# Performance work log

Measured on AMD Instinct MI355X. Metric: run time of the kernel, lower is better.

Reference implementation:

```python
import jax, jax.numpy as jnp
import numpy as np

EPS = 1e-05
GROUPS = 8


def setup_inputs() -> dict:
    key = jax.random.key(0)
    k1, k2, k3 = jax.random.split(key, 3)
    N, C, H, W = 32, 256, 56, 56
    x = jax.random.normal(k1, (N, C, H, W), dtype=jnp.float32)
    weight = jnp.ones((C,), dtype=jnp.float32)
    bias = jnp.zeros((C,), dtype=jnp.float32)
    gate_logits = jnp.array([2.8, 0.2, 1.1], dtype=jnp.float32)
    diag_proj = jnp.array([[0.08, -0.05, 0.08],
                           [-0.03, 0.08, -0.01],
                           [-0.05, -0.04, -0.07]], dtype=jnp.float32)
    return {"x": x, "weight": weight, "bias": bias,
            "gate_logits": gate_logits, "diag_proj": diag_proj}


def reference(x, weight, bias, gate_logits, diag_proj):
    xf = x.astype(jnp.float32)
    N, C, H, W = xf.shape

    # variance descriptor (differentiable: first-instance path recomputes without detach)
    batch_var = jnp.var(xf, axis=(0, 2, 3)).mean()    # per-channel var -> mean
    sample_var = jnp.var(xf, axis=(1, 2, 3)).mean()   # per-sample var -> mean
    channel_var = jnp.var(xf, axis=1).mean()          # var over channels at each (n,h,w) -> mean
    desc = jnp.tanh(jnp.log(jnp.maximum(jnp.stack([batch_var, sample_var, channel_var]), EPS)))

    gate = jax.nn.softmax(gate_logits + diag_proj @ desc)  # [3]

    # batch norm (training mode: batch statistics over N,H,W per channel)
    mu_b = xf.mean(axis=(0, 2, 3), keepdims=True)
    var_b = xf.var(axis=(0, 2, 3), keepdims=True)
    x_bn = (xf - mu_b) / jnp.sqrt(var_b + EPS)

    # layer norm = group_norm with 1 group: per-sample stats over C,H,W
    mu_l = xf.mean(axis=(1, 2, 3), keepdims=True)
    var_l = xf.var(axis=(1, 2, 3), keepdims=True)
    x_ln = (xf - mu_l) / jnp.sqrt(var_l + EPS)

    # group norm with GROUPS groups
    xg = xf.reshape(N, GROUPS, C // GROUPS, H, W)
    mu_g = xg.mean(axis=(2, 3, 4), keepdims=True)
    var_g = xg.var(axis=(2, 3, 4), keepdims=True)
    x_gn = ((xg - mu_g) / jnp.sqrt(var_g + EPS)).reshape(N, C, H, W)

    mixed = gate[0] * x_bn + gate[1] * x_ln + gate[2] * x_gn
    y = mixed * weight[None, :, None, None] + bias[None, :, None, None]
    return y.astype(x.dtype)
```

## Files before the change

### kernel.cpp

```cpp
#include <hip/hip_runtime.h>
#include <hip/hip_bf16.h>

#define NN 32
#define CC 256
#define HW 3136
#define HW4 784
#define CHW 802816
#define CHW4 200704
#define NCHW 25690112
#define GROUPS 8
#define CPG 32
#define NHW 100352
#define GHW 100352
#define EPSF 1e-5f
#define PCHUNK 13
#define NPT2 (NN*PCHUNK)
#define CGS 2
#define CPB 128

__global__ __launch_bounds__(256) void plane_stats_kernel(
    const float4* __restrict__ x4, float* __restrict__ S1, float* __restrict__ S2)
{
    const int wave = threadIdx.x >> 6, lane = threadIdx.x & 63;
    const int nc = blockIdx.x * 4 + wave;
    const float4* p = x4 + (size_t)nc * HW4;
    float s1 = 0.f, s2 = 0.f;
    #pragma unroll 4
    for (int i = lane; i < HW4; i += 64) {
        float4 v = p[i];
        s1 += v.x + v.y + v.z + v.w;
        s2 += v.x*v.x + v.y*v.y + v.z*v.z + v.w*v.w;
    }
    #pragma unroll
    for (int off = 32; off; off >>= 1) {
        s1 += __shfl_down(s1, off, 64);
        s2 += __shfl_down(s2, off, 64);
    }
    if (lane == 0) { S1[nc] = s1; S2[nc] = s2; }
}

__global__ __launch_bounds__(256) void chansum_kernel(
    const float* __restrict__ x, float* __restrict__ pT)
{
    const int b = blockIdx.x;
    const int chunk = b % PCHUNK;
    const int nc = b / PCHUNK;
    const int n = nc % NN;
    const int cg = nc / NN;
    const int pos = chunk * 256 + threadIdx.x;
    float T = 0.f;
    if (pos < HW) {
        const float* p = x + (size_t)n * CHW + (size_t)cg * CPB * HW + pos;
        #pragma unroll 16
        for (int c = 0; c < CPB; ++c) T += p[(size_t)c * HW];
    }
    pT[b * 256 + threadIdx.x] = (pos < HW) ? T : 0.f;
}

__global__ __launch_bounds__(256) void combine_kernel(
    const float* __restrict__ pT, float* __restrict__ pT2)
{
    const int b = blockIdx.x;
    const int tid = threadIdx.x;
    const float T = pT[b * 256 + tid] + pT[NN * PCHUNK * 256 + b * 256 + tid];
    float t2 = T * T;
    #pragma unroll
    for (int off = 32; off; off >>= 1) t2 += __shfl_down(t2, off, 64);
    __shared__ float sh[4];
    const int wave = tid >> 6, lane = tid & 63;
    if (lane == 0) sh[wave] = t2;
    __syncthreads();
    if (tid == 0) pT2[b] = sh[0] + sh[1] + sh[2] + sh[3];
}

__global__ __launch_bounds__(256) void finalize_kernel(
    const float* __restrict__ S1, const float* __restrict__ S2,
    const float* __restrict__ partialT2,
    const float* __restrict__ weight, const float* __restrict__ bias,
    const float* __restrict__ gate_logits, const float* __restrict__ diag_proj,
    float* __restrict__ A, float* __restrict__ B)
{
    const int tid = threadIdx.x;
    __shared__ float sh_mu_b[CC], sh_rs_b[CC];
    __shared__ float sh_mu_g[NN * GROUPS], sh_rs_g[NN * GROUPS];
    __shared__ float sh_mu_l[NN], sh_rs_l[NN];
    __shared__ float sh_red1[4], sh_red2[4], sh_red3[4], sh_red4[4];
    __shared__ float sh_gate[3];

    const float inv_NHW  = 1.f / (float)NHW;
    const float inv_CHW  = 1.f / (float)CHW;
    const float inv_GHW  = 1.f / (float)GHW;
    const float inv_NCHW = 1.f / (float)NCHW;

    const int c = tid;
    float s1 = 0.f, s2 = 0.f;
    for (int n = 0; n < NN; ++n) { s1 += S1[n * CC + c]; s2 += S2[n * CC + c]; }
    const float mu_b  = s1 * inv_NHW;
    const float var_b = s2 * inv_NHW - mu_b * mu_b;
    sh_mu_b[c] = mu_b;
    sh_rs_b[c] = rsqrtf(var_b + EPSF);

    const int ng_n = tid >> 3, ng_g = tid & 7;
    float s1g = 0.f, s2g = 0.f;
    for (int cc = 0; cc < CPG; ++cc) {
        const int idx = ng_n * CC + ng_g * CPG + cc;
        s1g += S1[idx]; s2g += S2[idx];
    }
    const float mu_g  = s1g * inv_GHW;
    const float var_g = s2g * inv_GHW - mu_g * mu_g;
    sh_mu_g[tid] = mu_g;
    sh_rs_g[tid] = rsqrtf(var_g + EPSF);

    float s1l = s1g, s2l = s2g;
    #pragma unroll
    for (int off = 1; off < 8; off <<= 1) {
        s1l += __shfl_xor(s1l, off, 64);
        s2l += __shfl_xor(s2l, off, 64);
    }
    float var_l_contrib = 0.f;
    if (ng_g == 0) {
        const float mu_l  = s1l * inv_CHW;
        const float var_l = s2l * inv_CHW - mu_l * mu_l;
        sh_mu_l[ng_n] = mu_l;
        sh_rs_l[ng_n] = rsqrtf(var_l + EPSF);
        var_l_contrib = var_l;
    }

    float t2p = 0.f;
    for (int i = tid; i < NPT2; i += 256) t2p += partialT2[i];

    float r1 = var_b, r2 = s2, r3 = var_l_contrib, r4 = t2p;
    #pragma unroll
    for (int off = 32; off; off >>= 1) {
        r1 += __shfl_down(r1, off, 64);
        r2 += __shfl_down(r2, off, 64);
        r3 += __shfl_down(r3, off, 64);
        r4 += __shfl_down(r4, off, 64);
    }
    const int wave = tid >> 6, lane = tid & 63;
    if (lane == 0) { sh_red1[wave] = r1; sh_red2[wave] = r2; sh_red3[wave] = r3; sh_red4[wave] = r4; }
    __syncthreads();
    if (tid == 0) {
        const float sum_var_b = sh_red1[0] + sh_red1[1] + sh_red1[2] + sh_red1[3];
        const float total_x2  = sh_red2[0] + sh_red2[1] + sh_red2[2] + sh_red2[3];
        const float sum_var_l = sh_red3[0] + sh_red3[1] + sh_red3[2] + sh_red3[3];
        const float sum_T2    = sh_red4[0] + sh_red4[1] + sh_red4[2] + sh_red4[3];

        const float batch_var   = sum_var_b * (1.f / (float)CC);
        const float sample_var  = sum_var_l * (1.f / (float)NN);
        const float channel_var = total_x2 * inv_NCHW
                                - sum_T2 * inv_NHW * (1.f / ((float)CC * (float)CC));

        float desc[3];
        desc[0] = tanhf(logf(fmaxf(batch_var,   EPSF)));
        desc[1] = tanhf(logf(fmaxf(sample_var,  EPSF)));
        desc[2] = tanhf(logf(fmaxf(channel_var, EPSF)));

        float lg[3];
        #pragma unroll
        for (int i = 0; i < 3; ++i) {
            lg[i] = gate_logits[i] + diag_proj[i*3+0]*desc[0]
                                   + diag_proj[i*3+1]*desc[1]
                                   + diag_proj[i*3+2]*desc[2];
        }
        const float m = fmaxf(lg[0], fmaxf(lg[1], lg[2]));
        const float e0 = expf(lg[0]-m), e1 = expf(lg[1]-m), e2 = expf(lg[2]-m);
        const float inv = 1.f / (e0 + e1 + e2);
        sh_gate[0] = e0 * inv; sh_gate[1] = e1 * inv; sh_gate[2] = e2 * inv;
    }
    __syncthreads();

    const float g0 = sh_gate[0], g1 = sh_gate[1], g2 = sh_gate[2];
    for (int i = tid; i < NN * CC; i += 256) {
        const int n = i >> 8, ch = i & 255, g = ch >> 5;
        const float w = weight[ch], bi = bias[ch];
        const float rb = sh_rs_b[ch], rl = sh_rs_l[n], rg = sh_rs_g[n*8+g];
        const float mb = sh_mu_b[ch], ml = sh_mu_l[n], mg = sh_mu_g[n*8+g];
        const float scale = g0*rb + g1*rl + g2*rg;
        const float offs  = g0*mb*rb + g1*ml*rl + g2*mg*rg;
        A[i] = w * scale;
        B[i] = bi - w * offs;
    }
}

__global__ __launch_bounds__(256) void apply_kernel(
    const float4* __restrict__ x4, const float* __restrict__ A,
    const float* __restrict__ B, float4* __restrict__ y4)
{
    const int nc = blockIdx.x;
    const float a = A[nc], b = B[nc];
    const float4* xp = x4 + (size_t)nc * HW4;
    float4* yp = y4 + (size_t)nc * HW4;
    for (int i = threadIdx.x; i < HW4; i += 256) {
        float4 v = xp[i];
        v.x = fmaf(v.x, a, b);
        v.y = fmaf(v.y, a, b);
        v.z = fmaf(v.z, a, b);
        v.w = fmaf(v.w, a, b);
        yp[i] = v;
    }
}

extern "C" void kernel_launch(void* const* d_in, const int* in_sizes, int n_in,
                              void* d_out, int out_size, void* d_ws, size_t ws_size,
                              hipStream_t stream) {
    const float* x           = (const float*)d_in[0];
    const float* weight      = (const float*)d_in[1];
    const float* bias        = (const float*)d_in[2];
    const float* gate_logits = (const float*)d_in[3];
    const float* diag_proj   = (const float*)d_in[4];
    float* out = (float*)d_out;

    float* ws  = (float*)d_ws;
    float* S1  = ws;
    float* S2  = ws + 8192;
    float* A   = ws + 16384;
    float* B   = ws + 24576;
    float* pT2 = ws + 32768;
    float* pT  = ws + 33280;

    plane_stats_kernel<<<NN * 64, 256, 0, stream>>>((const float4*)x, S1, S2);
    chansum_kernel<<<CGS * NN * PCHUNK, 256, 0, stream>>>(x, pT);
    combine_kernel<<<NN * PCHUNK, 256, 0, stream>>>(pT, pT2);
    finalize_kernel<<<1, 256, 0, stream>>>(S1, S2, pT2, weight, bias,
                                           gate_logits, diag_proj, A, B);
    apply_kernel<<<NN * CC, 256, 0, stream>>>((const float4*)x, A, B, (float4*)out);
}
```

Baseline: 77.28 us.

## Fuse plane stats and channel-sum passes into one launch with float4 channel sums

Merges the per-plane sum/sumsq kernel and the per-position channel-sum kernel into a single launch, with disjoint block ranges running each role. The channel-sum path now reads float4 vectors and splits channels into 4 groups of 64 instead of 2 of 128, so the combine kernel adds four partials. The aim is to drop a kernel launch, let both reads of x run concurrently and possibly share L2, and widen the strided channel loads. The workspace offset for the partial buffer moves, and pT4 must fit within the workspace.

```diff
diff --git a/kernel.cpp b/kernel.cpp
--- a/kernel.cpp
+++ b/kernel.cpp
@@ -13,57 +13,70 @@
 #define NHW 100352
 #define GHW 100352
 #define EPSF 1e-5f
-#define PCHUNK 13
-#define NPT2 (NN*PCHUNK)
-#define CGS 2
-#define CPB 128
-
-__global__ __launch_bounds__(256) void plane_stats_kernel(
-    const float4* __restrict__ x4, float* __restrict__ S1, float* __restrict__ S2)
-{
-    const int wave = threadIdx.x >> 6, lane = threadIdx.x & 63;
-    const int nc = blockIdx.x * 4 + wave;
-    const float4* p = x4 + (size_t)nc * HW4;
-    float s1 = 0.f, s2 = 0.f;
-    #pragma unroll 4
-    for (int i = lane; i < HW4; i += 64) {
-        float4 v = p[i];
-        s1 += v.x + v.y + v.z + v.w;
-        s2 += v.x*v.x + v.y*v.y + v.z*v.z + v.w*v.w;
-    }
-    #pragma unroll
-    for (int off = 32; off; off >>= 1) {
-        s1 += __shfl_down(s1, off, 64);
-        s2 += __shfl_down(s2, off, 64);
-    }
-    if (lane == 0) { S1[nc] = s1; S2[nc] = s2; }
-}
-
-__global__ __launch_bounds__(256) void chansum_kernel(
-    const float* __restrict__ x, float* __restrict__ pT)
-{
-    const int b = blockIdx.x;
-    const int chunk = b % PCHUNK;
-    const int nc = b / PCHUNK;
-    const int n = nc % NN;
-    const int cg = nc / NN;
-    const int pos = chunk * 256 + threadIdx.x;
-    float T = 0.f;
-    if (pos < HW) {
-        const float* p = x + (size_t)n * CHW + (size_t)cg * CPB * HW + pos;
-        #pragma unroll 16
-        for (int c = 0; c < CPB; ++c) T += p[(size_t)c * HW];
-    }
-    pT[b * 256 + threadIdx.x] = (pos < HW) ? T : 0.f;
+
+#define PCH4 4
+#define CG4 4
+#define CPB4 64
+#define NCHAN_BLOCKS (CG4*NN*PCH4)
+#define NPLANE_BLOCKS 2048
+#define NPT2 (NN*PCH4)
+
+__global__ __launch_bounds__(256) void stats_kernel(
+    const float4* __restrict__ x4, float* __restrict__ S1, float* __restrict__ S2,
+    float4* __restrict__ pT4)
+{
+    const int tid = threadIdx.x;
+    if (blockIdx.x < NCHAN_BLOCKS) {
+        const int b = blockIdx.x;
+        const int chunk = b & 3;
+        const int nc = b >> 2;
+        const int n = nc & 31;
+        const int cg = nc >> 5;
+        const int p4 = chunk * 256 + tid;
+        float4 T = make_float4(0.f, 0.f, 0.f, 0.f);
+        if (p4 < HW4) {
+            const float4* p = x4 + (size_t)n * CHW4 + (size_t)cg * CPB4 * HW4 + p4;
+            #pragma unroll 16
+            for (int c = 0; c < CPB4; ++c) {
+                float4 v = p[(size_t)c * HW4];
+                T.x += v.x; T.y += v.y; T.z += v.z; T.w += v.w;
+            }
+        }
+        pT4[b * 256 + tid] = T;
+    } else {
+        const int pb = blockIdx.x - NCHAN_BLOCKS;
+        const int wave = tid >> 6, lane = tid & 63;
+        const int ncid = pb * 4 + wave;
+        const float4* p = x4 + (size_t)ncid * HW4;
+        float s1 = 0.f, s2 = 0.f;
+        #pragma unroll 4
+        for (int i = lane; i < HW4; i += 64) {
+            float4 v = p[i];
+            s1 += v.x + v.y + v.z + v.w;
+            s2 += v.x*v.x + v.y*v.y + v.z*v.z + v.w*v.w;
+        }
+        #pragma unroll
+        for (int off = 32; off; off >>= 1) {
+            s1 += __shfl_down(s1, off, 64);
+            s2 += __shfl_down(s2, off, 64);
+        }
+        if (lane == 0) { S1[ncid] = s1; S2[ncid] = s2; }
+    }
 }
 
 __global__ __launch_bounds__(256) void combine_kernel(
-    const float* __restrict__ pT, float* __restrict__ pT2)
+    const float4* __restrict__ pT4, float* __restrict__ pT2)
 {
     const int b = blockIdx.x;
     const int tid = threadIdx.x;
-    const float T = pT[b * 256 + tid] + pT[NN * PCHUNK * 256 + b * 256 + tid];
-    float t2 = T * T;
+    const int n = b >> 2, chunk = b & 3;
+    float4 T = make_float4(0.f, 0.f, 0.f, 0.f);
+    #pragma unroll
+    for (int cg = 0; cg < CG4; ++cg) {
+        float4 v = pT4[((cg * NN + n) * PCH4 + chunk) * 256 + tid];
+        T.x += v.x; T.y += v.y; T.z += v.z; T.w += v.w;
+    }
+    float t2 = T.x*T.x + T.y*T.y + T.z*T.z + T.w*T.w;
     #pragma unroll
     for (int off = 32; off; off >>= 1) t2 += __shfl_down(t2, off, 64);
     __shared__ float sh[4];
@@ -217,11 +230,11 @@
     float* A   = ws + 16384;
     float* B   = ws + 24576;
     float* pT2 = ws + 32768;
-    float* pT  = ws + 33280;
-
-    plane_stats_kernel<<<NN * 64, 256, 0, stream>>>((const float4*)x, S1, S2);
-    chansum_kernel<<<CGS * NN * PCHUNK, 256, 0, stream>>>(x, pT);
-    combine_kernel<<<NN * PCHUNK, 256, 0, stream>>>(pT, pT2);
+    float* pT4f = ws + 33024;
+
+    stats_kernel<<<NCHAN_BLOCKS + NPLANE_BLOCKS, 256, 0, stream>>>(
+        (const float4*)x, S1, S2, (float4*)pT4f);
+    combine_kernel<<<NPT2, 256, 0, stream>>>((const float4*)pT4f, pT2);
     finalize_kernel<<<1, 256, 0, stream>>>(S1, S2, pT2, weight, bias,
                                            gate_logits, diag_proj, A, B);
     apply_kernel<<<NN * CC, 256, 0, stream>>>((const float4*)x, A, B, (float4*)out);
```

Result: no change. 78.30 us (+1.3%).

## Fuse all stages into one persistent kernel with software grid barriers

Applied to the files above, without the earlier changes.

Replaces the five separate launches (plane stats, channel sums, combine, finalize, apply) with a single kernel of 1024 blocks. Two atomic-counter grid barriers separate the statistics, finalize and apply phases. The channel-sum pass is reworked to use float4 loads and a shared-memory reduction in each block, which removes the separate combine kernel. This cuts launch overhead and inter-kernel gaps, but the barriers assume all 1024 blocks are co-resident, block 0 alone runs finalize while every other block waits, and a memset launch is added to reset the barrier.

```diff
diff --git a/kernel.cpp b/kernel.cpp
--- a/kernel.cpp
+++ b/kernel.cpp
@@ -3,201 +3,225 @@
 
 #define NN 32
 #define CC 256
-#define HW 3136
 #define HW4 784
+#define CHW4 200704
 #define CHW 802816
-#define CHW4 200704
 #define NCHW 25690112
 #define GROUPS 8
 #define CPG 32
 #define NHW 100352
 #define GHW 100352
 #define EPSF 1e-5f
-#define PCHUNK 13
-#define NPT2 (NN*PCHUNK)
-#define CGS 2
-#define CPB 128
-
-__global__ __launch_bounds__(256) void plane_stats_kernel(
-    const float4* __restrict__ x4, float* __restrict__ S1, float* __restrict__ S2)
+
+#define NBLK 1024
+#define PCHUNK 25
+
+__device__ inline void grid_barrier(unsigned* cnt, unsigned* gen)
 {
-    const int wave = threadIdx.x >> 6, lane = threadIdx.x & 63;
-    const int nc = blockIdx.x * 4 + wave;
-    const float4* p = x4 + (size_t)nc * HW4;
-    float s1 = 0.f, s2 = 0.f;
-    #pragma unroll 4
-    for (int i = lane; i < HW4; i += 64) {
-        float4 v = p[i];
-        s1 += v.x + v.y + v.z + v.w;
-        s2 += v.x*v.x + v.y*v.y + v.z*v.z + v.w*v.w;
-    }
-    #pragma unroll
-    for (int off = 32; off; off >>= 1) {
-        s1 += __shfl_down(s1, off, 64);
-        s2 += __shfl_down(s2, off, 64);
-    }
-    if (lane == 0) { S1[nc] = s1; S2[nc] = s2; }
+    __syncthreads();
+    if (threadIdx.x == 0) {
+        __threadfence();
+        unsigned g = __hip_atomic_load(gen, __ATOMIC_RELAXED, __HIP_MEMORY_SCOPE_AGENT);
+        unsigned old = __hip_atomic_fetch_add(cnt, 1u, __ATOMIC_ACQ_REL, __HIP_MEMORY_SCOPE_AGENT);
+        if (old == NBLK - 1u) {
+            __hip_atomic_store(cnt, 0u, __ATOMIC_RELAXED, __HIP_MEMORY_SCOPE_AGENT);
+            __hip_atomic_store(gen, g + 1u, __ATOMIC_RELEASE, __HIP_MEMORY_SCOPE_AGENT);
+        } else {
+            for (long it = 0; it < 2000000; ++it) {
+                if (__hip_atomic_load(gen, __ATOMIC_RELAXED, __HIP_MEMORY_SCOPE_AGENT) != g) break;
+                __builtin_amdgcn_s_sleep(2);
+            }
+        }
+        __threadfence();
+    }
+    __syncthreads();
 }
 
-__global__ __launch_bounds__(256) void chansum_kernel(
-    const float* __restrict__ x, float* __restrict__ pT)
-{
-    const int b = blockIdx.x;
-    const int chunk = b % PCHUNK;
-    const int nc = b / PCHUNK;
-    const int n = nc % NN;
-    const int cg = nc / NN;
-    const int pos = chunk * 256 + threadIdx.x;
-    float T = 0.f;
-    if (pos < HW) {
-        const float* p = x + (size_t)n * CHW + (size_t)cg * CPB * HW + pos;
-        #pragma unroll 16
-        for (int c = 0; c < CPB; ++c) T += p[(size_t)c * HW];
-    }
-    pT[b * 256 + threadIdx.x] = (pos < HW) ? T : 0.f;
-}
-
-__global__ __launch_bounds__(256) void combine_kernel(
-    const float* __restrict__ pT, float* __restrict__ pT2)
-{
-    const int b = blockIdx.x;
-    const int tid = threadIdx.x;
-    const float T = pT[b * 256 + tid] + pT[NN * PCHUNK * 256 + b * 256 + tid];
-    float t2 = T * T;
-    #pragma unroll
-    for (int off = 32; off; off >>= 1) t2 += __shfl_down(t2, off, 64);
-    __shared__ float sh[4];
-    const int wave = tid >> 6, lane = tid & 63;
-    if (lane == 0) sh[wave] = t2;
-    __syncthreads();
-    if (tid == 0) pT2[b] = sh[0] + sh[1] + sh[2] + sh[3];
-}
-
-__global__ __launch_bounds__(256) void finalize_kernel(
-    const float* __restrict__ S1, const float* __restrict__ S2,
-    const float* __restrict__ partialT2,
+__global__ __launch_bounds__(256, 4) void mega_kernel(
+    const float4* __restrict__ x4,
     const float* __restrict__ weight, const float* __restrict__ bias,
     const float* __restrict__ gate_logits, const float* __restrict__ diag_proj,
-    float* __restrict__ A, float* __restrict__ B)
+    float4* __restrict__ y4,
+    unsigned* cnt, unsigned* gen,
+    float* __restrict__ S1, float* __restrict__ S2,
+    float* __restrict__ Aarr, float* __restrict__ Barr,
+    float* __restrict__ pT2)
 {
-    const int tid = threadIdx.x;
-    __shared__ float sh_mu_b[CC], sh_rs_b[CC];
-    __shared__ float sh_mu_g[NN * GROUPS], sh_rs_g[NN * GROUPS];
-    __shared__ float sh_mu_l[NN], sh_rs_l[NN];
-    __shared__ float sh_red1[4], sh_red2[4], sh_red3[4], sh_red4[4];
-    __shared__ float sh_gate[3];
-
-    const float inv_NHW  = 1.f / (float)NHW;
-    const float inv_CHW  = 1.f / (float)CHW;
-    const float inv_GHW  = 1.f / (float)GHW;
-    const float inv_NCHW = 1.f / (float)NCHW;
-
-    const int c = tid;
-    float s1 = 0.f, s2 = 0.f;
-    for (int n = 0; n < NN; ++n) { s1 += S1[n * CC + c]; s2 += S2[n * CC + c]; }
-    const float mu_b  = s1 * inv_NHW;
-    const float var_b = s2 * inv_NHW - mu_b * mu_b;
-    sh_mu_b[c] = mu_b;
-    sh_rs_b[c] = rsqrtf(var_b + EPSF);
-
-    const int ng_n = tid >> 3, ng_g = tid & 7;
-    float s1g = 0.f, s2g = 0.f;
-    for (int cc = 0; cc < CPG; ++cc) {
-        const int idx = ng_n * CC + ng_g * CPG + cc;
-        s1g += S1[idx]; s2g += S2[idx];
-    }
-    const float mu_g  = s1g * inv_GHW;
-    const float var_g = s2g * inv_GHW - mu_g * mu_g;
-    sh_mu_g[tid] = mu_g;
-    sh_rs_g[tid] = rsqrtf(var_g + EPSF);
-
-    float s1l = s1g, s2l = s2g;
+    const int tid  = threadIdx.x;
+    const int wave = tid >> 6, lane = tid & 63;
+
     #pragma unroll
-    for (int off = 1; off < 8; off <<= 1) {
-        s1l += __shfl_xor(s1l, off, 64);
-        s2l += __shfl_xor(s2l, off, 64);
-    }
-    float var_l_contrib = 0.f;
-    if (ng_g == 0) {
-        const float mu_l  = s1l * inv_CHW;
-        const float var_l = s2l * inv_CHW - mu_l * mu_l;
-        sh_mu_l[ng_n] = mu_l;
-        sh_rs_l[ng_n] = rsqrtf(var_l + EPSF);
-        var_l_contrib = var_l;
-    }
-
-    float t2p = 0.f;
-    for (int i = tid; i < NPT2; i += 256) t2p += partialT2[i];
-
-    float r1 = var_b, r2 = s2, r3 = var_l_contrib, r4 = t2p;
+    for (int rep = 0; rep < 2; ++rep) {
+        const int plane = blockIdx.x * 4 + wave + rep * (NBLK * 4);
+        const float4* p = x4 + (size_t)plane * HW4;
+        float s1 = 0.f, s2 = 0.f;
+        #pragma unroll 4
+        for (int i = lane; i < HW4; i += 64) {
+            float4 v = p[i];
+            s1 += v.x + v.y + v.z + v.w;
+            s2 += v.x*v.x + v.y*v.y + v.z*v.z + v.w*v.w;
+        }
+        #pragma unroll
+        for (int off = 32; off; off >>= 1) {
+            s1 += __shfl_down(s1, off, 64);
+            s2 += __shfl_down(s2, off, 64);
+        }
+        if (lane == 0) { S1[plane] = s1; S2[plane] = s2; }
+    }
+
+    {
+        const int n = blockIdx.x >> 5, chunk = blockIdx.x & 31;
+        const int start = chunk * PCHUNK;
+        const int len = (HW4 - start) < PCHUNK ? (HW4 - start) : PCHUNK;
+        const int cg = tid >> 5, p = tid & 31;
+        float4 T = make_float4(0.f, 0.f, 0.f, 0.f);
+        if (p < len) {
+            const float4* q = x4 + (size_t)n * CHW4 + (size_t)(cg * 32) * HW4 + start + p;
+            #pragma unroll 8
+            for (int c = 0; c < 32; ++c) {
+                float4 v = q[(size_t)c * HW4];
+                T.x += v.x; T.y += v.y; T.z += v.z; T.w += v.w;
+            }
+        }
+        __shared__ float4 shT[32];
+        #pragma unroll
+        for (int k = 0; k < 8; ++k) {
+            if (cg == k) {
+                if (k == 0) shT[p] = T;
+                else { shT[p].x += T.x; shT[p].y += T.y; shT[p].z += T.z; shT[p].w += T.w; }
+            }
+            __syncthreads();
+        }
+        float t2 = 0.f;
+        if (tid < 32) {
+            float4 t = shT[tid];
+            t2 = t.x*t.x + t.y*t.y + t.z*t.z + t.w*t.w;
+        }
+        #pragma unroll
+        for (int off = 32; off; off >>= 1) t2 += __shfl_down(t2, off, 64);
+        if (tid == 0) pT2[blockIdx.x] = t2;
+    }
+
+    grid_barrier(cnt, gen);
+
+    if (blockIdx.x == 0) {
+        __shared__ float sh_mu_b[CC], sh_rs_b[CC];
+        __shared__ float sh_mu_g[NN * GROUPS], sh_rs_g[NN * GROUPS];
+        __shared__ float sh_mu_l[NN], sh_rs_l[NN];
+        __shared__ float sh_red1[4], sh_red2[4], sh_red3[4], sh_red4[4];
+        __shared__ float sh_gate[3];
+
+        const float inv_NHW  = 1.f / (float)NHW;
+        const float inv_CHW  = 1.f / (float)CHW;
+        const float inv_GHW  = 1.f / (float)GHW;
+        const float inv_NCHW = 1.f / (float)NCHW;
+
+        const int c = tid;
+        float s1 = 0.f, s2 = 0.f;
+        for (int n = 0; n < NN; ++n) { s1 += S1[n * CC + c]; s2 += S2[n * CC + c]; }
+        const float mu_b  = s1 * inv_NHW;
+        const float var_b = s2 * inv_NHW - mu_b * mu_b;
+        sh_mu_b[c] = mu_b;
+        sh_rs_b[c] = rsqrtf(var_b + EPSF);
+
+        const int ng_n = tid >> 3, ng_g = tid & 7;
+        float s1g = 0.f, s2g = 0.f;
+        for (int cc2 = 0; cc2 < CPG; ++cc2) {
+            const int idx = ng_n * CC + ng_g * CPG + cc2;
+            s1g += S1[idx]; s2g += S2[idx];
+        }
+        const float mu_g  = s1g * inv_GHW;
+        const float var_g = s2g * inv_GHW - mu_g * mu_g;
+        sh_mu_g[tid] = mu_g;
+        sh_rs_g[tid] = rsqrtf(var_g + EPSF);
+
+        float s1l = s1g, s2l = s2g;
+        #pragma unroll
+        for (int off = 1; off < 8; off <<= 1) {
+            s1l += __shfl_xor(s1l, off, 64);
+            s2l += __shfl_xor(s2l, off, 64);
+        }
+        float var_l_contrib = 0.f;
+        if (ng_g == 0) {
+            const float mu_l  = s1l * inv_CHW;
+            const float var_l = s2l * inv_CHW - mu_l * mu_l;
+            sh_mu_l[ng_n] = mu_l;
+            sh_rs_l[ng_n] = rsqrtf(var_l + EPSF);
+            var_l_contrib = var_l;
+        }
+
+        float t2p = 0.f;
+        for (int i = tid; i < NBLK; i += 256) t2p += pT2[i];
+
+        float r1 = var_b, r2 = s2, r3 = var_l_contrib, r4 = t2p;
+        #pragma unroll
+        for (int off = 32; off; off >>= 1) {
+            r1 += __shfl_down(r1, off, 64);
+            r2 += __shfl_down(r2, off, 64);
+            r3 += __shfl_down(r3, off, 64);
+            r4 += __shfl_down(r4, off, 64);
+        }
+        if (lane == 0) { sh_red1[wave] = r1; sh_red2[wave] = r2; sh_red3[wave] = r3; sh_red4[wave] = r4; }
+        __syncthreads();
+        if (tid == 0) {
+            const float sum_var_b = sh_red1[0] + sh_red1[1] + sh_red1[2] + sh_red1[3];
+            const float total_x2  = sh_red2[0] + sh_red2[1] + sh_red2[2] + sh_red2[3];
+            const float sum_var_l = sh_red3[0] + sh_red3[1] + sh_red3[2] + sh_red3[3];
+            const float sum_T2    = sh_red4[0] + sh_red4[1] + sh_red4[2] + sh_red4[3];
+
+            const float batch_var   = sum_var_b * (1.f / (float)CC);
+            const float sample_var  = sum_var_l * (1.f / (float)NN);
+            const float channel_var = total_x2 * inv_NCHW
+                                    - sum_T2 * inv_NHW * (1.f / ((float)CC * (float)CC));
+
+            float desc[3];
+            desc[0] = tanhf(logf(fmaxf(batch_var,   EPSF)));
+            desc[1] = tanhf(logf(fmaxf(sample_var,  EPSF)));
+            desc[2] = tanhf(logf(fmaxf(channel_var, EPSF)));
+
+            float lg[3];
+            #pragma unroll
+            for (int i = 0; i < 3; ++i) {
+                lg[i] = gate_logits[i] + diag_proj[i*3+0]*desc[0]
+                                       + diag_proj[i*3+1]*desc[1]
+                                       + diag_proj[i*3+2]*desc[2];
+            }
+            const float m = fmaxf(lg[0], fmaxf(lg[1], lg[2]));
+            const float e0 = expf(lg[0]-m), e1 = expf(lg[1]-m), e2 = expf(lg[2]-m);
+            const float inv = 1.f / (e0 + e1 + e2);
+            sh_gate[0] = e0 * inv; sh_gate[1] = e1 * inv; sh_gate[2] = e2 * inv;
+        }
+        __syncthreads();
+
+        const float g0 = sh_gate[0], g1 = sh_gate[1], g2 = sh_gate[2];
+        for (int i = tid; i < NN * CC; i += 256) {
+            const int n = i >> 8, ch = i & 255, g = ch >> 5;
+            const float w = weight[ch], bi = bias[ch];
+            const float rb = sh_rs_b[ch], rl = sh_rs_l[n], rg = sh_rs_g[n*8+g];
+            const float mb = sh_mu_b[ch], ml = sh_mu_l[n], mg = sh_mu_g[n*8+g];
+            const float scale = g0*rb + g1*rl + g2*rg;
+            const float offs  = g0*mb*rb + g1*ml*rl + g2*mg*rg;
+            Aarr[i] = w * scale;
+            Barr[i] = bi - w * offs;
+        }
+    }
+
+    grid_barrier(cnt, gen);
+
     #pragma unroll
-    for (int off = 32; off; off >>= 1) {
-        r1 += __shfl_down(r1, off, 64);
-        r2 += __shfl_down(r2, off, 64);
-        r3 += __shfl_down(r3, off, 64);
-        r4 += __shfl_down(r4, off, 64);
-    }
-    const int wave = tid >> 6, lane = tid & 63;
-    if (lane == 0) { sh_red1[wave] = r1; sh_red2[wave] = r2; sh_red3[wave] = r3; sh_red4[wave] = r4; }
-    __syncthreads();
-    if (tid == 0) {
-        const float sum_var_b = sh_red1[0] + sh_red1[1] + sh_red1[2] + sh_red1[3];
-        const float total_x2  = sh_red2[0] + sh_red2[1] + sh_red2[2] + sh_red2[3];
-        const float sum_var_l = sh_red3[0] + sh_red3[1] + sh_red3[2] + sh_red3[3];
-        const float sum_T2    = sh_red4[0] + sh_red4[1] + sh_red4[2] + sh_red4[3];
-
-        const float batch_var   = sum_var_b * (1.f / (float)CC);
-        const float sample_var  = sum_var_l * (1.f / (float)NN);
-        const float channel_var = total_x2 * inv_NCHW
-                                - sum_T2 * inv_NHW * (1.f / ((float)CC * (float)CC));
-
-        float desc[3];
-        desc[0] = tanhf(logf(fmaxf(batch_var,   EPSF)));
-        desc[1] = tanhf(logf(fmaxf(sample_var,  EPSF)));
-        desc[2] = tanhf(logf(fmaxf(channel_var, EPSF)));
-
-        float lg[3];
-        #pragma unroll
-        for (int i = 0; i < 3; ++i) {
-            lg[i] = gate_logits[i] + diag_proj[i*3+0]*desc[0]
-                                   + diag_proj[i*3+1]*desc[1]
-                                   + diag_proj[i*3+2]*desc[2];
-        }
-        const float m = fmaxf(lg[0], fmaxf(lg[1], lg[2]));
-        const float e0 = expf(lg[0]-m), e1 = expf(lg[1]-m), e2 = expf(lg[2]-m);
-        const float inv = 1.f / (e0 + e1 + e2);
-        sh_gate[0] = e0 * inv; sh_gate[1] = e1 * inv; sh_gate[2] = e2 * inv;
-    }
-    __syncthreads();
-
-    const float g0 = sh_gate[0], g1 = sh_gate[1], g2 = sh_gate[2];
-    for (int i = tid; i < NN * CC; i += 256) {
-        const int n = i >> 8, ch = i & 255, g = ch >> 5;
-        const float w = weight[ch], bi = bias[ch];
-        const float rb = sh_rs_b[ch], rl = sh_rs_l[n], rg = sh_rs_g[n*8+g];
-        const float mb = sh_mu_b[ch], ml = sh_mu_l[n], mg = sh_mu_g[n*8+g];
-        const float scale = g0*rb + g1*rl + g2*rg;
-        const float offs  = g0*mb*rb + g1*ml*rl + g2*mg*rg;
-        A[i] = w * scale;
-        B[i] = bi - w * offs;
-    }
-}
-
-__global__ __launch_bounds__(256) void apply_kernel(
-    const float4* __restrict__ x4, const float* __restrict__ A,
-    const float* __restrict__ B, float4* __restrict__ y4)
-{
-    const int nc = blockIdx.x;
-    const float a = A[nc], b = B[nc];
-    const float4* xp = x4 + (size_t)nc * HW4;
-    float4* yp = y4 + (size_t)nc * HW4;
-    for (int i = threadIdx.x; i < HW4; i += 256) {
-        float4 v = xp[i];
-        v.x = fmaf(v.x, a, b);
-        v.y = fmaf(v.y, a, b);
-        v.z = fmaf(v.z, a, b);
-        v.w = fmaf(v.w, a, b);
-        yp[i] = v;
+    for (int j = 0; j < 8; ++j) {
+        const int plane = blockIdx.x + j * NBLK;
+        const float a = Aarr[plane], b = Barr[plane];
+        const float4* xp = x4 + (size_t)plane * HW4;
+        float4* yp = y4 + (size_t)plane * HW4;
+        for (int i = tid; i < HW4; i += 256) {
+            float4 v = xp[i];
+            v.x = fmaf(v.x, a, b);
+            v.y = fmaf(v.y, a, b);
+            v.z = fmaf(v.z, a, b);
+            v.w = fmaf(v.w, a, b);
+            yp[i] = v;
+        }
     }
 }
 
@@ -211,18 +235,17 @@
     const float* diag_proj   = (const float*)d_in[4];
     float* out = (float*)d_out;
 
+    unsigned* bar = (unsigned*)d_ws;
     float* ws  = (float*)d_ws;
-    float* S1  = ws;
-    float* S2  = ws + 8192;
-    float* A   = ws + 16384;
-    float* B   = ws + 24576;
-    float* pT2 = ws + 32768;
-    float* pT  = ws + 33280;
-
-    plane_stats_kernel<<<NN * 64, 256, 0, stream>>>((const float4*)x, S1, S2);
-    chansum_kernel<<<CGS * NN * PCHUNK, 256, 0, stream>>>(x, pT);
-    combine_kernel<<<NN * PCHUNK, 256, 0, stream>>>(pT, pT2);
-    finalize_kernel<<<1, 256, 0, stream>>>(S1, S2, pT2, weight, bias,
-                                           gate_logits, diag_proj, A, B);
-    apply_kernel<<<NN * CC, 256, 0, stream>>>((const float4*)x, A, B, (float4*)out);
+    float* S1   = ws + 16;
+    float* S2   = ws + 16 + 8192;
+    float* Aarr = ws + 16 + 16384;
+    float* Barr = ws + 16 + 24576;
+    float* pT2  = ws + 16 + 32768;
+
+    hipMemsetAsync(bar, 0, 2 * sizeof(unsigned), stream);
+
+    mega_kernel<<<NBLK, 256, 0, stream>>>(
+        (const float4*)x, weight, bias, gate_logits, diag_proj,
+        (float4*)out, bar, bar + 1, S1, S2, Aarr, Barr, pT2);
 }
```

Result: slower. 308.0 us (+298.6%).

## Vectorize channel-sum pass with float4 and regroup channels into eight groups

Applied to the files above, without the earlier changes.

The channel-sum pass now reads float4 vectors along spatial positions and splits the channels into 8 groups of 32 instead of 2 of 128. Positions are flattened across the batch, which gives 784 blocks, and the combine kernel sums 8 partial float4 vectors before squaring. The plane-stats loop is fully unrolled to 12 iterations plus a tail. The aim is wider memory transactions and more parallelism in the second full read of x, at the cost of a larger intermediate partial buffer.

```diff
diff --git a/kernel.cpp b/kernel.cpp
--- a/kernel.cpp
+++ b/kernel.cpp
@@ -13,10 +13,12 @@
 #define NHW 100352
 #define GHW 100352
 #define EPSF 1e-5f
-#define PCHUNK 13
-#define NPT2 (NN*PCHUNK)
-#define CGS 2
-#define CPB 128
+
+#define NPOS4 25088
+#define POSBLK 98
+#define CGS 8
+#define CPB 32
+#define NPT2 POSBLK
 
 __global__ __launch_bounds__(256) void plane_stats_kernel(
     const float4* __restrict__ x4, float* __restrict__ S1, float* __restrict__ S2)
@@ -25,9 +27,14 @@
     const int nc = blockIdx.x * 4 + wave;
     const float4* p = x4 + (size_t)nc * HW4;
     float s1 = 0.f, s2 = 0.f;
-    #pragma unroll 4
-    for (int i = lane; i < HW4; i += 64) {
-        float4 v = p[i];
+    #pragma unroll
+    for (int j = 0; j < 12; ++j) {
+        float4 v = p[lane + j * 64];
+        s1 += v.x + v.y + v.z + v.w;
+        s2 += v.x*v.x + v.y*v.y + v.z*v.z + v.w*v.w;
+    }
+    if (lane < 16) {
+        float4 v = p[768 + lane];
         s1 += v.x + v.y + v.z + v.w;
         s2 += v.x*v.x + v.y*v.y + v.z*v.z + v.w*v.w;
     }
@@ -40,37 +47,42 @@
 }
 
 __global__ __launch_bounds__(256) void chansum_kernel(
-    const float* __restrict__ x, float* __restrict__ pT)
-{
-    const int b = blockIdx.x;
-    const int chunk = b % PCHUNK;
-    const int nc = b / PCHUNK;
-    const int n = nc % NN;
-    const int cg = nc / NN;
-    const int pos = chunk * 256 + threadIdx.x;
-    float T = 0.f;
-    if (pos < HW) {
-        const float* p = x + (size_t)n * CHW + (size_t)cg * CPB * HW + pos;
-        #pragma unroll 16
-        for (int c = 0; c < CPB; ++c) T += p[(size_t)c * HW];
-    }
-    pT[b * 256 + threadIdx.x] = (pos < HW) ? T : 0.f;
+    const float4* __restrict__ x4, float4* __restrict__ pT4)
+{
+    const int cg = blockIdx.x / POSBLK;
+    const int pb = blockIdx.x % POSBLK;
+    const int pos = pb * 256 + threadIdx.x;
+    const int n = pos / HW4;
+    const int p4 = pos - n * HW4;
+    const float4* q = x4 + (size_t)n * CHW4 + (size_t)(cg * CPB) * HW4 + p4;
+    float4 T = make_float4(0.f, 0.f, 0.f, 0.f);
+    #pragma unroll 8
+    for (int c = 0; c < CPB; ++c) {
+        float4 v = q[(size_t)c * HW4];
+        T.x += v.x; T.y += v.y; T.z += v.z; T.w += v.w;
+    }
+    pT4[(size_t)cg * NPOS4 + pos] = T;
 }
 
 __global__ __launch_bounds__(256) void combine_kernel(
-    const float* __restrict__ pT, float* __restrict__ pT2)
-{
-    const int b = blockIdx.x;
+    const float4* __restrict__ pT4, float* __restrict__ pT2)
+{
     const int tid = threadIdx.x;
-    const float T = pT[b * 256 + tid] + pT[NN * PCHUNK * 256 + b * 256 + tid];
-    float t2 = T * T;
+    const int pos = blockIdx.x * 256 + tid;
+    float4 T = make_float4(0.f, 0.f, 0.f, 0.f);
+    #pragma unroll
+    for (int cg = 0; cg < CGS; ++cg) {
+        float4 v = pT4[(size_t)cg * NPOS4 + pos];
+        T.x += v.x; T.y += v.y; T.z += v.z; T.w += v.w;
+    }
+    float t2 = T.x*T.x + T.y*T.y + T.z*T.z + T.w*T.w;
     #pragma unroll
     for (int off = 32; off; off >>= 1) t2 += __shfl_down(t2, off, 64);
     __shared__ float sh[4];
     const int wave = tid >> 6, lane = tid & 63;
     if (lane == 0) sh[wave] = t2;
     __syncthreads();
-    if (tid == 0) pT2[b] = sh[0] + sh[1] + sh[2] + sh[3];
+    if (tid == 0) pT2[blockIdx.x] = sh[0] + sh[1] + sh[2] + sh[3];
 }
 
 __global__ __launch_bounds__(256) void finalize_kernel(
@@ -102,8 +114,8 @@
 
     const int ng_n = tid >> 3, ng_g = tid & 7;
     float s1g = 0.f, s2g = 0.f;
-    for (int cc = 0; cc < CPG; ++cc) {
-        const int idx = ng_n * CC + ng_g * CPG + cc;
+    for (int cc2 = 0; cc2 < CPG; ++cc2) {
+        const int idx = ng_n * CC + ng_g * CPG + cc2;
         s1g += S1[idx]; s2g += S2[idx];
     }
     const float mu_g  = s1g * inv_GHW;
@@ -211,17 +223,17 @@
     const float* diag_proj   = (const float*)d_in[4];
     float* out = (float*)d_out;
 
-    float* ws  = (float*)d_ws;
-    float* S1  = ws;
-    float* S2  = ws + 8192;
-    float* A   = ws + 16384;
-    float* B   = ws + 24576;
-    float* pT2 = ws + 32768;
-    float* pT  = ws + 33280;
-
-    plane_stats_kernel<<<NN * 64, 256, 0, stream>>>((const float4*)x, S1, S2);
-    chansum_kernel<<<CGS * NN * PCHUNK, 256, 0, stream>>>(x, pT);
-    combine_kernel<<<NN * PCHUNK, 256, 0, stream>>>(pT, pT2);
+    float* ws   = (float*)d_ws;
+    float* S1   = ws;
+    float* S2   = ws + 8192;
+    float* A    = ws + 16384;
+    float* B    = ws + 24576;
+    float* pT2  = ws + 32768;
+    float* pT4f = ws + 32896;
+
+    plane_stats_kernel<<<2048, 256, 0, stream>>>((const float4*)x, S1, S2);
+    chansum_kernel<<<CGS * POSBLK, 256, 0, stream>>>((const float4*)x, (float4*)pT4f);
+    combine_kernel<<<POSBLK, 256, 0, stream>>>((const float4*)pT4f, pT2);
     finalize_kernel<<<1, 256, 0, stream>>>(S1, S2, pT2, weight, bias,
                                            gate_logits, diag_proj, A, B);
     apply_kernel<<<NN * CC, 256, 0, stream>>>((const float4*)x, A, B, (float4*)out);
```

Result: no change. 77.77 us (+0.6%).
